# Optimization experiments

Hardware: AMD Instinct MI355X
Metric: run time of the kernel (lower is better)

Reference implementation:

```python
import jax, jax.numpy as jnp
import numpy as np

D_MODEL = 256
D_HID = 128
EPS = 1e-5
MASK_VALUE = -10000.0


def _layer_norm(x, scale, bias):
    mu = jnp.mean(x, axis=-1, keepdims=True)
    var = jnp.mean(jnp.square(x - mu), axis=-1, keepdims=True)
    return (x - mu) * jax.lax.rsqrt(var + EPS) * scale + bias


def setup_inputs() -> dict:
    key = jax.random.key(0)
    ks = jax.random.split(key, 8)
    B, S = 32, 1024
    std = 0.02
    return {
        "x": jax.random.normal(ks[0], (B, S, D_MODEL), dtype=jnp.float32),
        "ln1_scale": jnp.ones((D_MODEL,), jnp.float32),
        "ln1_bias": jnp.zeros((D_MODEL,), jnp.float32),
        "w_qkv": jax.random.normal(ks[1], (D_MODEL, 3 * D_MODEL), jnp.float32) * std,
        "b_qkv": jnp.zeros((3 * D_MODEL,), jnp.float32),
        "w_proj": jax.random.normal(ks[2], (D_MODEL, D_MODEL), jnp.float32) * std,
        "b_proj": jnp.zeros((D_MODEL,), jnp.float32),
        "ln2_scale": jnp.ones((D_MODEL,), jnp.float32),
        "ln2_bias": jnp.zeros((D_MODEL,), jnp.float32),
        "w_fc1": jax.random.normal(ks[3], (D_MODEL, D_HID), jnp.float32) * std,
        "b_fc1": jnp.zeros((D_HID,), jnp.float32),
        "w_fc2": jax.random.normal(ks[4], (D_HID, D_MODEL), jnp.float32) * std,
        "b_fc2": jnp.zeros((D_MODEL,), jnp.float32),
    }


def reference(x, ln1_scale, ln1_bias, w_qkv, b_qkv, w_proj, b_proj,
              ln2_scale, ln2_bias, w_fc1, b_fc1, w_fc2, b_fc2):
    B, S, D = x.shape
    # --- pre-LN self-attention ---
    residual = x
    h = _layer_norm(x, ln1_scale, ln1_bias)
    qkv = h @ w_qkv + b_qkv                       # [B, S, 3D]
    q, k, v = jnp.split(qkv, 3, axis=2)           # each [B, S, D]; 1 head, head_dim=D
    scale = 1.0 / jnp.sqrt(jnp.asarray(D, x.dtype))
    scores = jnp.einsum('bqd,bkd->bqk', q, k) * scale   # [B, S, S]
    causal = jnp.tril(jnp.ones((S, S), dtype=bool))
    scores = jnp.where(causal[None, :, :], scores, MASK_VALUE)
    attn = jax.nn.softmax(scores, axis=-1)        # dropout is identity (eval mode)
    out = jnp.einsum('bqk,bkd->bqd', attn, v)     # [B, S, D]
    out = out @ w_proj + b_proj
    x = out + residual
    # --- pre-LN MLP ---
    residual = x
    h = _layer_norm(x, ln2_scale, ln2_bias)
    h = jax.nn.relu(h @ w_fc1 + b_fc1)
    h = h @ w_fc2 + b_fc2
    return h + residual
```

## Files before the change

### kernel.cpp

```cpp
#include <hip/hip_runtime.h>
#include <hip/hip_bf16.h>

#define D_MODEL 256
#define D_HID   128
#define SEQ     1024
#define NBATCH  32
#define NROWS   (NBATCH * SEQ)
#define MASKV   -10000.0f
#define EPSLN   1e-5f

typedef unsigned short u16;
using bf16x8 = __attribute__((ext_vector_type(8))) short;
using f32x4  = __attribute__((ext_vector_type(4))) float;

union U8 { uint4 v; u16 s[8]; };

__device__ __forceinline__ float bf2f(u16 u) {
    unsigned int x = ((unsigned int)u) << 16;
    return __uint_as_float(x);
}
__device__ __forceinline__ u16 f2bf(float f) {
    unsigned int u = __float_as_uint(f);
    u += 0x7fff + ((u >> 16) & 1);
    return (u16)(u >> 16);
}
__device__ __forceinline__ void load4(const float* p, float* f) {
    float4 a = *(const float4*)p;
    f[0] = a.x; f[1] = a.y; f[2] = a.z; f[3] = a.w;
}
__device__ __forceinline__ void load4(const u16* p, float* f) {
    ushort4 v = *(const ushort4*)p;
    f[0] = bf2f(v.x); f[1] = bf2f(v.y); f[2] = bf2f(v.z); f[3] = bf2f(v.w);
}
__device__ __forceinline__ void gload16(const u16* g, u16* l) {
    __builtin_amdgcn_global_load_lds(
        (const __attribute__((address_space(1))) void*)g,
        (__attribute__((address_space(3))) void*)l, 16, 0, 0);
}

template <int CTRL>
__device__ __forceinline__ float dpp_mov(float v) {
    return __int_as_float(__builtin_amdgcn_update_dpp(
        0, __float_as_int(v), CTRL, 0xf, 0xf, true));
}
__device__ __forceinline__ float red16_max(float v) {
    v = fmaxf(v, dpp_mov<0xB1>(v));
    v = fmaxf(v, dpp_mov<0x4E>(v));
    v = fmaxf(v, dpp_mov<0x141>(v));
    v = fmaxf(v, dpp_mov<0x140>(v));
    return v;
}
__device__ __forceinline__ float red16_sum(float v) {
    v += dpp_mov<0xB1>(v);
    v += dpp_mov<0x4E>(v);
    v += dpp_mov<0x141>(v);
    v += dpp_mov<0x140>(v);
    return v;
}

__global__ __launch_bounds__(256) void transpose_weights(
    const float* __restrict__ wqkv, u16* __restrict__ wqkvT,
    const float* __restrict__ wproj, u16* __restrict__ wprojT,
    const float* __restrict__ wfc1, u16* __restrict__ wfc1T,
    const float* __restrict__ wfc2, u16* __restrict__ wfc2T) {
    int tid = blockIdx.x * 256 + threadIdx.x;
    int stride = gridDim.x * 256;
    for (int i = tid; i < 768 * 256; i += stride) {
        int n = i >> 8, k = i & 255;
        wqkvT[i] = f2bf(wqkv[k * 768 + n]);
    }
    for (int i = tid; i < 256 * 256; i += stride) {
        int n = i >> 8, k = i & 255;
        wprojT[i] = f2bf(wproj[k * 256 + n]);
    }
    for (int i = tid; i < 128 * 256; i += stride) {
        int n = i >> 8, k = i & 255;
        wfc1T[i] = f2bf(wfc1[k * 128 + n]);
    }
    for (int i = tid; i < 256 * 128; i += stride) {
        int n = i >> 7, k = i & 127;
        wfc2T[i] = f2bf(wfc2[k * 256 + n]);
    }
}

template <typename TX>
__global__ __launch_bounds__(256) void ln_fused(
    const TX* __restrict__ x, const float* __restrict__ gamma,
    const float* __restrict__ beta, u16* __restrict__ out) {
    int wave = threadIdx.x >> 6, lane = threadIdx.x & 63;
    int row = blockIdx.x * 4 + wave;
    float f[4];
    load4(x + (size_t)row * D_MODEL + lane * 4, f);
    float s  = f[0] + f[1] + f[2] + f[3];
    float sq = f[0] * f[0] + f[1] * f[1] + f[2] * f[2] + f[3] * f[3];
    #pragma unroll
    for (int off = 1; off < 64; off <<= 1) {
        s  += __shfl_xor(s, off);
        sq += __shfl_xor(sq, off);
    }
    float mu   = s * (1.0f / 256.0f);
    float var  = sq * (1.0f / 256.0f) - mu * mu;
    float rstd = rsqrtf(var + EPSLN);
    float g[4], be[4];
    load4(gamma + lane * 4, g);
    load4(beta + lane * 4, be);
    ushort4 o;
    o.x = f2bf((f[0] - mu) * rstd * g[0] + be[0]);
    o.y = f2bf((f[1] - mu) * rstd * g[1] + be[1]);
    o.z = f2bf((f[2] - mu) * rstd * g[2] + be[2]);
    o.w = f2bf((f[3] - mu) * rstd * g[3] + be[3]);
    *(ushort4*)(out + (size_t)row * D_MODEL + lane * 4) = o;
}

#define GT2_ELEMS (2 * 128 * 128)

template <int K>
__device__ __forceinline__ void gemm_tile2(
    const u16* __restrict__ A, const u16* __restrict__ BT,
    int m0, int n0, u16* lds, f32x4 acc[4][4]) {
    u16* ldsA = lds;
    u16* ldsB = lds + 128 * 128;
    const int tid = threadIdx.x;
    const int lane = tid & 63, wave = tid >> 6;
    const int wr = (wave >> 1) * 64, wc = (wave & 1) * 64;
    const int row = lane & 15, quad = lane >> 4;

    for (int ks = 0; ks < K; ks += 128) {
        __syncthreads();
        #pragma unroll
        for (int i = 0; i < 8; i++) {
            int blk = i * 4 + wave;
            int B = (blk << 10) + lane * 16;
            int r = B >> 8;
            int cb = (B & 255) ^ ((r & 7) << 4);
            gload16(A + (size_t)(m0 + r) * K + ks + (cb >> 1),
                    ldsA + (blk << 9));
            gload16(BT + (size_t)(n0 + r) * K + ks + (cb >> 1),
                    ldsB + (blk << 9));
        }
        __syncthreads();
        #pragma unroll
        for (int k0 = 0; k0 < 128; k0 += 32) {
            bf16x8 a[4], b[4];
            #pragma unroll
            for (int mi = 0; mi < 4; mi++) {
                int rr = wr + mi * 16 + row;
                a[mi] = *(const bf16x8*)(ldsA + rr * 128 +
                         ((k0 + quad * 8) ^ ((rr & 7) << 3)));
            }
            #pragma unroll
            for (int nj = 0; nj < 4; nj++) {
                int rr = wc + nj * 16 + row;
                b[nj] = *(const bf16x8*)(ldsB + rr * 128 +
                         ((k0 + quad * 8) ^ ((rr & 7) << 3)));
            }
            #pragma unroll
            for (int mi = 0; mi < 4; mi++)
                #pragma unroll
                for (int nj = 0; nj < 4; nj++)
                    acc[mi][nj] = __builtin_amdgcn_mfma_f32_16x16x32_bf16(
                        a[mi], b[nj], acc[mi][nj], 0, 0, 0);
        }
    }
}

#define ZERO_ACC4(acc)                                       \
    _Pragma("unroll") for (int i_ = 0; i_ < 4; i_++)         \
    _Pragma("unroll") for (int j_ = 0; j_ < 4; j_++)         \
    _Pragma("unroll") for (int e_ = 0; e_ < 4; e_++) acc[i_][j_][e_] = 0.0f;

#define EPILOG_IDX4                                          \
    int lane = threadIdx.x & 63, wave = threadIdx.x >> 6;    \
    int wr = (wave >> 1) * 64, wc = (wave & 1) * 64;         \
    int row = lane & 15, quad = lane >> 4;

__global__ __launch_bounds__(256) void gemm_qkv(
    const u16* __restrict__ h, const u16* __restrict__ wqkvT,
    const float* __restrict__ b_qkv,
    u16* __restrict__ q, u16* __restrict__ kk, u16* __restrict__ vT) {
    __shared__ u16 lds[GT2_ELEMS];
    f32x4 acc[4][4];
    ZERO_ACC4(acc)
    int m0 = blockIdx.x * 128, n0 = blockIdx.y * 128;
    gemm_tile2<256>(h, wqkvT, m0, n0, lds, acc);
    EPILOG_IDX4
    #pragma unroll
    for (int mi = 0; mi < 4; mi++) {
        #pragma unroll
        for (int nj = 0; nj < 4; nj++) {
            int gn = n0 + wc + nj * 16 + row;
            float bias = b_qkv[gn];
            int gm = m0 + wr + mi * 16 + quad * 4;
            if (gn < 256) {
                #pragma unroll
                for (int r = 0; r < 4; r++)
                    q[(size_t)(gm + r) * 256 + gn] =
                        f2bf((acc[mi][nj][r] + bias) * 0.0625f);
            } else if (gn < 512) {
                int col = gn - 256;
                #pragma unroll
                for (int r = 0; r < 4; r++)
                    kk[(size_t)(gm + r) * 256 + col] = f2bf(acc[mi][nj][r] + bias);
            } else {
                int d = gn - 512;
                int b = gm >> 10, s = gm & 1023;
                ushort4 pack;
                pack.x = f2bf(acc[mi][nj][0] + bias);
                pack.y = f2bf(acc[mi][nj][1] + bias);
                pack.z = f2bf(acc[mi][nj][2] + bias);
                pack.w = f2bf(acc[mi][nj][3] + bias);
                *(ushort4*)(vT + ((size_t)(b * 256 + d) << 10) + s) = pack;
            }
        }
    }
}

__global__ __launch_bounds__(256) void gemm_proj(
    const u16* __restrict__ ao, const u16* __restrict__ wprojT,
    const float* __restrict__ b_proj, const float* __restrict__ x_in,
    u16* __restrict__ x2) {
    __shared__ u16 lds[GT2_ELEMS];
    f32x4 acc[4][4];
    ZERO_ACC4(acc)
    int m0 = blockIdx.x * 128, n0 = blockIdx.y * 128;
    gemm_tile2<256>(ao, wprojT, m0, n0, lds, acc);
    EPILOG_IDX4
    #pragma unroll
    for (int mi = 0; mi < 4; mi++)
        #pragma unroll
        for (int nj = 0; nj < 4; nj++) {
            int gn = n0 + wc + nj * 16 + row;
            float bias = b_proj[gn];
            int gm = m0 + wr + mi * 16 + quad * 4;
            #pragma unroll
            for (int r = 0; r < 4; r++) {
                size_t idx = (size_t)(gm + r) * 256 + gn;
                x2[idx] = f2bf(acc[mi][nj][r] + bias + x_in[idx]);
            }
        }
}

__global__ __launch_bounds__(256) void gemm_mlp(
    const u16* __restrict__ x2, const float* __restrict__ g2,
    const float* __restrict__ be2,
    const u16* __restrict__ wfc1T, const float* __restrict__ b_fc1,
    const u16* __restrict__ wfc2T, const float* __restrict__ b_fc2,
    float* __restrict__ out) {
    __shared__ u16 lds[65536];
    u16* ldsB1 = lds + 32768;
    u16* ldsA1 = lds + 49152;
    const int tid = threadIdx.x;
    const int lane = tid & 63, wave = tid >> 6;
    const int rowl = lane & 15, quad = lane >> 4;
    const int wr = (wave >> 1) * 64, wc = (wave & 1) * 64;
    const int m0 = blockIdx.x * 128;

    #pragma unroll
    for (int i = 0; i < 16; i++) {
        int blk = i * 4 + wave;
        int B = (blk << 10) + lane * 16;
        int r = B >> 9;
        int cb = (B & 511) ^ ((r & 7) << 4);
        gload16(x2 + (size_t)(m0 + r) * 256 + (cb >> 1), lds + (B >> 1));
    }
    #pragma unroll
    for (int i = 0; i < 8; i++) {
        int blk = i * 4 + wave;
        int B = (blk << 10) + lane * 16;
        int r = B >> 8;
        int cb = (B & 255) ^ ((r & 7) << 4);
        gload16(wfc1T + (size_t)r * 256 + 0 + (cb >> 1), ldsB1 + (B >> 1));
    }
    __syncthreads();

    {
        float4 g4  = *(const float4*)(g2 + lane * 4);
        float4 be4 = *(const float4*)(be2 + lane * 4);
        #pragma unroll 4
        for (int i = 0; i < 32; i++) {
            int r = wave + i * 4;
            char* p = (char*)lds + r * 512 + ((lane * 8) ^ ((r & 7) << 4));
            ushort4 v = *(ushort4*)p;
            float f0 = bf2f(v.x), f1 = bf2f(v.y), f2v = bf2f(v.z), f3 = bf2f(v.w);
            float s  = f0 + f1 + f2v + f3;
            float sq = f0*f0 + f1*f1 + f2v*f2v + f3*f3;
            s = red16_sum(s);   s += __shfl_xor(s, 16);   s += __shfl_xor(s, 32);
            sq = red16_sum(sq); sq += __shfl_xor(sq, 16); sq += __shfl_xor(sq, 32);
            float mu   = s * (1.0f / 256.0f);
            float var  = sq * (1.0f / 256.0f) - mu * mu;
            float rstd = rsqrtf(var + EPSLN);
            ushort4 o;
            o.x = f2bf((f0  - mu) * rstd * g4.x + be4.x);
            o.y = f2bf((f1  - mu) * rstd * g4.y + be4.y);
            o.z = f2bf((f2v - mu) * rstd * g4.z + be4.z);
            o.w = f2bf((f3  - mu) * rstd * g4.w + be4.w);
            *(ushort4*)p = o;
        }
    }
    __syncthreads();

    f32x4 acc1[4][4];
    ZERO_ACC4(acc1)
    #pragma unroll
    for (int ks = 0; ks < 256; ks += 128) {
        if (ks) {
            __syncthreads();
            #pragma unroll
            for (int i = 0; i < 8; i++) {
                int blk = i * 4 + wave;
                int B = (blk << 10) + lane * 16;
                int r = B >> 8;
                int cb = (B & 255) ^ ((r & 7) << 4);
                gload16(wfc1T + (size_t)r * 256 + ks + (cb >> 1),
                        ldsB1 + (B >> 1));
            }
            __syncthreads();
        }
        #pragma unroll
        for (int k0 = 0; k0 < 128; k0 += 32) {
            bf16x8 a[4], b[4];
            #pragma unroll
            for (int mi = 0; mi < 4; mi++) {
                int rr = wr + mi * 16 + rowl;
                a[mi] = *(const bf16x8*)((const char*)lds + rr * 512 +
                         ((((ks + k0 + quad * 8) << 1)) ^ ((rr & 7) << 4)));
            }
            #pragma unroll
            for (int nj = 0; nj < 4; nj++) {
                int rb = wc + nj * 16 + rowl;
                b[nj] = *(const bf16x8*)((const char*)ldsB1 + rb * 256 +
                         ((((k0 + quad * 8) << 1)) ^ ((rb & 7) << 4)));
            }
            #pragma unroll
            for (int mi = 0; mi < 4; mi++)
                #pragma unroll
                for (int nj = 0; nj < 4; nj++)
                    acc1[mi][nj] = __builtin_amdgcn_mfma_f32_16x16x32_bf16(
                        a[mi], b[nj], acc1[mi][nj], 0, 0, 0);
        }
    }
    #pragma unroll
    for (int mi = 0; mi < 4; mi++)
        #pragma unroll
        for (int nj = 0; nj < 4; nj++) {
            int gn_l = wc + nj * 16 + rowl;
            float bias = b_fc1[gn_l];
            #pragma unroll
            for (int r = 0; r < 4; r++) {
                int gm_l = wr + mi * 16 + quad * 4 + r;
                *(u16*)((char*)ldsA1 + gm_l * 256 +
                        (((gn_l << 1)) ^ ((gm_l & 7) << 4))) =
                    f2bf(fmaxf(acc1[mi][nj][r] + bias, 0.0f));
            }
        }
    __syncthreads();

    #pragma unroll
    for (int i = 0; i < 16; i++) {
        int blk = i * 4 + wave;
        int B = (blk << 10) + lane * 16;
        int r = B >> 8;
        int cb = (B & 255) ^ ((r & 7) << 4);
        gload16(wfc2T + (size_t)r * 128 + (cb >> 1), lds + (B >> 1));
    }
    __syncthreads();

    const int wc2 = (wave & 1) * 128;
    f32x4 acc2[4][8];
    #pragma unroll
    for (int mi = 0; mi < 4; mi++)
        #pragma unroll
        for (int nj = 0; nj < 8; nj++)
            #pragma unroll
            for (int e = 0; e < 4; e++) acc2[mi][nj][e] = 0.0f;
    #pragma unroll
    for (int k0 = 0; k0 < 128; k0 += 32) {
        bf16x8 a[4], b[8];
        #pragma unroll
        for (int mi = 0; mi < 4; mi++) {
            int rr = wr + mi * 16 + rowl;
            a[mi] = *(const bf16x8*)((const char*)ldsA1 + rr * 256 +
                     ((((k0 + quad * 8) << 1)) ^ ((rr & 7) << 4)));
        }
        #pragma unroll
        for (int nj = 0; nj < 8; nj++) {
            int rb = wc2 + nj * 16 + rowl;
            b[nj] = *(const bf16x8*)((const char*)lds + rb * 256 +
                     ((((k0 + quad * 8) << 1)) ^ ((rb & 7) << 4)));
        }
        #pragma unroll
        for (int mi = 0; mi < 4; mi++)
            #pragma unroll
            for (int nj = 0; nj < 8; nj++)
                acc2[mi][nj] = __builtin_amdgcn_mfma_f32_16x16x32_bf16(
                    a[mi], b[nj], acc2[mi][nj], 0, 0, 0);
    }
    #pragma unroll
    for (int mi = 0; mi < 4; mi++)
        #pragma unroll
        for (int nj = 0; nj < 8; nj++) {
            int gn = wc2 + nj * 16 + rowl;
            float bias = b_fc2[gn];
            int gm = m0 + wr + mi * 16 + quad * 4;
            #pragma unroll
            for (int r = 0; r < 4; r++) {
                size_t idx = (size_t)(gm + r) * 256 + gn;
                out[idx] = acc2[mi][nj][r] + bias + bf2f(x2[idx]);
            }
        }
}

__constant__ unsigned char WQT[24] = {7,15,15,14,14,6,13,13,12,12,5,11,
                                      11,10,10,4,9,9,8,8,3,2,1,0};
__constant__ unsigned char WH[24]  = {2,0,1,0,1,2,0,1,0,1,2,0,
                                      1,0,1,2,0,1,0,1,2,2,2,2};

__global__ __launch_bounds__(256) void attn_kernel(
    const u16* __restrict__ q, const u16* __restrict__ k,
    const u16* __restrict__ vT, u16* __restrict__ ao,
    u16* __restrict__ part, float* __restrict__ ml) {
    __shared__ u16 k_lds[2][32 * 256];
    __shared__ u16 v_lds[2][256 * 32];
    __shared__ u16 p_lds[4][16 * 40];

    int j = blockIdx.x;
    int b = j & 31, w = j >> 5;
    int qt = WQT[w], hh = WH[w];
    int lo, hi;
    if (hh == 2) { lo = 0; hi = 2 * qt + 2; }
    else         { lo = hh * (qt + 1); hi = lo + qt + 1; }

    int tid = threadIdx.x;
    int lane = tid & 63, wave = tid >> 6;
    int row = lane & 15, quad = lane >> 4;
    int q0 = qt * 64;
    int qrow0 = q0 + wave * 16;

    const u16* qb = q + ((size_t)b << 10) * 256;
    const u16* kb = k + ((size_t)b << 10) * 256;
    const u16* vb = vT + (((size_t)b * 256) << 10);

    const int kxor = (row & 7) << 3;
    const int vxor = (row & 6) << 2;

    bf16x8 qf[8];
    #pragma unroll
    for (int kf = 0; kf < 8; kf++)
        qf[kf] = *(const bf16x8*)(qb + (size_t)(qrow0 + row) * 256 + kf * 32 + quad * 8);

    f32x4 o[16];
    #pragma unroll
    for (int n = 0; n < 16; n++)
        #pragma unroll
        for (int e = 0; e < 4; e++) o[n][e] = 0.0f;
    float m_i[4], l_i[4];
    #pragma unroll
    for (int r = 0; r < 4; r++) { m_i[r] = -1e30f; l_i[r] = 0.0f; }

    int wlast = 2 * qt + (wave >> 1);

    auto stage = [&](int bf, int kt) {
        int k0 = kt << 5;
        #pragma unroll
        for (int c = 0; c < 4; c++) {
            int blk = wave * 4 + c;
            int B = (blk << 10) + lane * 16;
            int rk = B >> 9;
            int ck = (B & 511) ^ ((rk & 7) << 4);
            gload16(kb + (size_t)(k0 + rk) * 256 + (ck >> 1),
                    &k_lds[bf][blk << 9]);
            int rv = B >> 6;
            int cv = (B & 63) ^ ((rv & 6) << 3);
            gload16(vb + ((size_t)rv << 10) + k0 + (cv >> 1),
                    &v_lds[bf][blk << 9]);
        }
    };

    stage(0, lo);
    __syncthreads();

    for (int kt = lo; kt < hi; kt++) {
        int cur = (kt - lo) & 1;
        if (kt + 1 < hi) stage(cur ^ 1, kt + 1);
        if (kt <= wlast) {
            const u16* kl = k_lds[cur];
            const u16* vl = v_lds[cur];

            f32x4 sf[2];
            #pragma unroll
            for (int jn = 0; jn < 2; jn++)
                #pragma unroll
                for (int e = 0; e < 4; e++) sf[jn][e] = 0.0f;
            __builtin_amdgcn_s_setprio(1);
            #pragma unroll
            for (int kf = 0; kf < 8; kf++)
                #pragma unroll
                for (int jn = 0; jn < 2; jn++) {
                    bf16x8 bfrag = *(const bf16x8*)(kl +
                        ((((jn * 16 + row) * 256) + kf * 32 + quad * 8) ^ kxor));
                    sf[jn] = __builtin_amdgcn_mfma_f32_16x16x32_bf16(
                        qf[kf], bfrag, sf[jn], 0, 0, 0);
                }
            __builtin_amdgcn_s_setprio(0);

            int kk0 = kt * 32;
            bool diag = (kt == wlast);
            int qrow = qrow0 + quad * 4;
            float sv[2][4];
            #pragma unroll
            for (int jn = 0; jn < 2; jn++)
                #pragma unroll
                for (int r = 0; r < 4; r++) {
                    float v = sf[jn][r];
                    if (diag && (kk0 + jn * 16 + row > qrow + r)) v = MASKV;
                    sv[jn][r] = v;
                }

            float pmax[4];
            int need = 0;
            #pragma unroll
            for (int r = 0; r < 4; r++) {
                pmax[r] = red16_max(fmaxf(sv[0][r], sv[1][r]));
                need |= (pmax[r] > m_i[r] + 8.0f) ? 1 : 0;
            }
            if (__any(need)) {
                #pragma unroll
                for (int r = 0; r < 4; r++) {
                    float mnew = fmaxf(m_i[r], pmax[r]);
                    float al = __expf(m_i[r] - mnew);
                    m_i[r] = mnew;
                    l_i[r] *= al;
                    #pragma unroll
                    for (int n = 0; n < 16; n++) o[n][r] *= al;
                }
            }
            #pragma unroll
            for (int r = 0; r < 4; r++) {
                float ps = 0.0f;
                #pragma unroll
                for (int jn = 0; jn < 2; jn++) {
                    sv[jn][r] = __expf(sv[jn][r] - m_i[r]);
                    ps += sv[jn][r];
                }
                l_i[r] += red16_sum(ps);
            }

            u16* pw = p_lds[wave];
            #pragma unroll
            for (int jn = 0; jn < 2; jn++)
                #pragma unroll
                for (int r = 0; r < 4; r++)
                    pw[(quad * 4 + r) * 40 + jn * 16 + row] = f2bf(sv[jn][r]);
            bf16x8 pf = *(const bf16x8*)(pw + row * 40 + quad * 8);

            __builtin_amdgcn_s_setprio(1);
            #pragma unroll
            for (int n = 0; n < 16; n++) {
                bf16x8 bv = *(const bf16x8*)(vl +
                    ((((n * 16 + row) * 32) + quad * 8) ^ vxor));
                o[n] = __builtin_amdgcn_mfma_f32_16x16x32_bf16(pf, bv, o[n], 0, 0, 0);
            }
            __builtin_amdgcn_s_setprio(0);
        }
        __syncthreads();
    }

    if (hh == 2) {
        float inv[4];
        #pragma unroll
        for (int r = 0; r < 4; r++) inv[r] = 1.0f / l_i[r];
        u16* aob = ao + (((size_t)b << 10) + qrow0) * 256;
        #pragma unroll
        for (int r = 0; r < 4; r++)
            #pragma unroll
            for (int n = 0; n < 16; n++)
                aob[(size_t)(quad * 4 + r) * 256 + n * 16 + row] =
                    f2bf(o[n][r] * inv[r]);
    } else {
        int p = (((b << 3) | (qt - 8)) << 1) | hh;
        u16* pb = part + (((size_t)p) << 6) * 256;
        #pragma unroll
        for (int r = 0; r < 4; r++) {
            int rt = wave * 16 + quad * 4 + r;
            #pragma unroll
            for (int n = 0; n < 16; n++)
                pb[(size_t)rt * 256 + n * 16 + row] = f2bf(o[n][r]);
        }
        if (row == 0) {
            #pragma unroll
            for (int r = 0; r < 4; r++) {
                int rt = wave * 16 + quad * 4 + r;
                float2 v2; v2.x = m_i[r]; v2.y = l_i[r];
                *(float2*)(ml + ((size_t)((p << 6) + rt)) * 2) = v2;
            }
        }
    }
}

__global__ __launch_bounds__(256) void attn_merge(
    const u16* __restrict__ part, const float* __restrict__ ml,
    u16* __restrict__ ao) {
    int j = blockIdx.x;
    int b = j >> 3, qi = j & 7;
    int t = threadIdx.x;
    int r = t >> 2, cq = t & 3;
    int pA = j << 1, pB = pA | 1;
    const float* mlA = ml + ((size_t)(pA << 6) + r) * 2;
    const float* mlB = ml + ((size_t)(pB << 6) + r) * 2;
    float mA = mlA[0], lA = mlA[1];
    float mB = mlB[0], lB = mlB[1];
    float m  = fmaxf(mA, mB);
    float eA = __expf(mA - m), eB = __expf(mB - m);
    float inv = 1.0f / (lA * eA + lB * eB);
    float sA = eA * inv, sB = eB * inv;
    const u16* oA = part + (((size_t)(pA << 6) + r) * 256) + cq * 64;
    const u16* oB = part + (((size_t)(pB << 6) + r) * 256) + cq * 64;
    u16* dst = ao + ((size_t)((b << 10) + 512 + (qi << 6) + r)) * 256 + cq * 64;
    #pragma unroll
    for (int u = 0; u < 8; u++) {
        U8 a, bb, o;
        a.v  = *(const uint4*)(oA + u * 8);
        bb.v = *(const uint4*)(oB + u * 8);
        #pragma unroll
        for (int e = 0; e < 8; e++)
            o.s[e] = f2bf(bf2f(a.s[e]) * sA + bf2f(bb.s[e]) * sB);
        *(uint4*)(dst + u * 8) = o.v;
    }
}

extern "C" void kernel_launch(void* const* d_in, const int* in_sizes, int n_in,
                              void* d_out, int out_size, void* d_ws, size_t ws_size,
                              hipStream_t stream) {
    const float* x      = (const float*)d_in[0];
    const float* ln1_s  = (const float*)d_in[1];
    const float* ln1_b  = (const float*)d_in[2];
    const float* w_qkv  = (const float*)d_in[3];
    const float* b_qkv  = (const float*)d_in[4];
    const float* w_proj = (const float*)d_in[5];
    const float* b_proj = (const float*)d_in[6];
    const float* ln2_s  = (const float*)d_in[7];
    const float* ln2_b  = (const float*)d_in[8];
    const float* w_fc1  = (const float*)d_in[9];
    const float* b_fc1  = (const float*)d_in[10];
    const float* w_fc2  = (const float*)d_in[11];
    const float* b_fc2  = (const float*)d_in[12];
    float* out = (float*)d_out;

    u16* h  = (u16*)d_out;
    u16* h2 = h + (size_t)NROWS * 256;

    u16* W = (u16*)d_ws;
    u16* wqkvT  = W;
    u16* wprojT = wqkvT + 196608;
    u16* wfc1T  = wprojT + 65536;
    u16* wfc2T  = wfc1T + 32768;
    u16* buf1   = wfc2T + 32768;
    u16* buf2   = buf1 + (size_t)NROWS * 256;
    u16* buf3   = buf2 + (size_t)NROWS * 256;

    u16*   part  = h;
    float* mlbuf = (float*)h2;

    transpose_weights<<<dim3(64), dim3(256), 0, stream>>>(
        w_qkv, wqkvT, w_proj, wprojT, w_fc1, wfc1T, w_fc2, wfc2T);
    ln_fused<float><<<dim3(NROWS / 4), dim3(256), 0, stream>>>(
        x, ln1_s, ln1_b, h);
    gemm_qkv<<<dim3(NROWS / 128, 6), dim3(256), 0, stream>>>(
        h, wqkvT, b_qkv, buf1, buf2, buf3);
    attn_kernel<<<dim3(768), dim3(256), 0, stream>>>(
        buf1, buf2, buf3, buf1, part, mlbuf);
    attn_merge<<<dim3(256), dim3(256), 0, stream>>>(
        part, mlbuf, buf1);
    gemm_proj<<<dim3(NROWS / 128, 2), dim3(256), 0, stream>>>(
        buf1, wprojT, b_proj, x, buf2);
    gemm_mlp<<<dim3(NROWS / 128), dim3(256), 0, stream>>>(
        buf2, ln2_s, ln2_b, wfc1T, b_fc1, wfc2T, b_fc2, out);
}
```

Measured before the change: 246.4 us.

## Use 128-row query tiles with 512-thread attention blocks and rebalance KV splits

Attention blocks now cover 128 query rows with 8 waves instead of 64 rows with 4, so each staged K/V tile is shared by twice as many query rows. Each thread stages half as many chunks. The work split changes: the first 128-row tile runs unsplit and all later tiles are split into two equal KV halves, giving 480 blocks. The merge kernel, the partial-buffer indexing and the placement of the ml buffer are rewritten to match. The aim is less K/V reload traffic and better load balance, at the cost of larger blocks, higher register pressure under launch_bounds(512,4), and more merge work.

After: 372.5 us. 1.51x slower.

```diff
diff --git a/kernel.cpp b/kernel.cpp
--- a/kernel.cpp
+++ b/kernel.cpp
@@ -410,31 +410,29 @@
         }
 }
 
-__constant__ unsigned char WQT[24] = {7,15,15,14,14,6,13,13,12,12,5,11,
-                                      11,10,10,4,9,9,8,8,3,2,1,0};
-__constant__ unsigned char WH[24]  = {2,0,1,0,1,2,0,1,0,1,2,0,
-                                      1,0,1,2,0,1,0,1,2,2,2,2};
-
-__global__ __launch_bounds__(256) void attn_kernel(
+__constant__ unsigned char CQT[15] = {7,6,6,5,5,4,4,7, 0,1,1,2,2,3,3};
+__constant__ unsigned char CH[15]  = {0,0,1,0,1,0,1,1, 2,0,1,0,1,0,1};
+
+__global__ __launch_bounds__(512, 4) void attn_kernel(
     const u16* __restrict__ q, const u16* __restrict__ k,
     const u16* __restrict__ vT, u16* __restrict__ ao,
     u16* __restrict__ part, float* __restrict__ ml) {
     __shared__ u16 k_lds[2][32 * 256];
     __shared__ u16 v_lds[2][256 * 32];
-    __shared__ u16 p_lds[4][16 * 40];
+    __shared__ u16 p_lds[8][16 * 40];
 
     int j = blockIdx.x;
-    int b = j & 31, w = j >> 5;
-    int qt = WQT[w], hh = WH[w];
+    int b = j & 31, c = j >> 5;
+    int qt = CQT[c], ch = CH[c];
+    int span = 2 * qt + 2;
     int lo, hi;
-    if (hh == 2) { lo = 0; hi = 2 * qt + 2; }
-    else         { lo = hh * (qt + 1); hi = lo + qt + 1; }
+    if (ch == 2) { lo = 0; hi = 4; }
+    else         { lo = ch * span; hi = lo + span; }
 
     int tid = threadIdx.x;
     int lane = tid & 63, wave = tid >> 6;
     int row = lane & 15, quad = lane >> 4;
-    int q0 = qt * 64;
-    int qrow0 = q0 + wave * 16;
+    int qrow0 = qt * 128 + wave * 16;
 
     const u16* qb = q + ((size_t)b << 10) * 256;
     const u16* kb = k + ((size_t)b << 10) * 256;
@@ -457,13 +455,13 @@
     #pragma unroll
     for (int r = 0; r < 4; r++) { m_i[r] = -1e30f; l_i[r] = 0.0f; }
 
-    int wlast = 2 * qt + (wave >> 1);
+    int wlast = 4 * qt + (wave >> 1);
 
     auto stage = [&](int bf, int kt) {
         int k0 = kt << 5;
         #pragma unroll
-        for (int c = 0; c < 4; c++) {
-            int blk = wave * 4 + c;
+        for (int cc = 0; cc < 2; cc++) {
+            int blk = wave * 2 + cc;
             int B = (blk << 10) + lane * 16;
             int rk = B >> 9;
             int ck = (B & 511) ^ ((rk & 7) << 4);
@@ -565,7 +563,7 @@
         __syncthreads();
     }
 
-    if (hh == 2) {
+    if (ch == 2) {
         float inv[4];
         #pragma unroll
         for (int r = 0; r < 4; r++) inv[r] = 1.0f / l_i[r];
@@ -577,8 +575,8 @@
                 aob[(size_t)(quad * 4 + r) * 256 + n * 16 + row] =
                     f2bf(o[n][r] * inv[r]);
     } else {
-        int p = (((b << 3) | (qt - 8)) << 1) | hh;
-        u16* pb = part + (((size_t)p) << 6) * 256;
+        int pq = b * 7 + (qt - 1);
+        u16* pb = part + ((size_t)(ch * 224 + pq) << 15);
         #pragma unroll
         for (int r = 0; r < 4; r++) {
             int rt = wave * 16 + quad * 4 + r;
@@ -587,11 +585,12 @@
                 pb[(size_t)rt * 256 + n * 16 + row] = f2bf(o[n][r]);
         }
         if (row == 0) {
+            int p = pq * 2 + ch;
             #pragma unroll
             for (int r = 0; r < 4; r++) {
                 int rt = wave * 16 + quad * 4 + r;
                 float2 v2; v2.x = m_i[r]; v2.y = l_i[r];
-                *(float2*)(ml + ((size_t)((p << 6) + rt)) * 2) = v2;
+                *(float2*)(ml + ((size_t)(p * 128 + rt)) * 2) = v2;
             }
         }
     }
@@ -601,21 +600,23 @@
     const u16* __restrict__ part, const float* __restrict__ ml,
     u16* __restrict__ ao) {
     int j = blockIdx.x;
-    int b = j >> 3, qi = j & 7;
+    int b = j / 14, rem = j - b * 14;
+    int qt = (rem >> 1) + 1, rh = rem & 1;
     int t = threadIdx.x;
     int r = t >> 2, cq = t & 3;
-    int pA = j << 1, pB = pA | 1;
-    const float* mlA = ml + ((size_t)(pA << 6) + r) * 2;
-    const float* mlB = ml + ((size_t)(pB << 6) + r) * 2;
+    int rt = rh * 64 + r;
+    int pq = b * 7 + (qt - 1);
+    const float* mlA = ml + ((size_t)((pq * 2 + 0) * 128 + rt)) * 2;
+    const float* mlB = ml + ((size_t)((pq * 2 + 1) * 128 + rt)) * 2;
     float mA = mlA[0], lA = mlA[1];
     float mB = mlB[0], lB = mlB[1];
     float m  = fmaxf(mA, mB);
     float eA = __expf(mA - m), eB = __expf(mB - m);
     float inv = 1.0f / (lA * eA + lB * eB);
     float sA = eA * inv, sB = eB * inv;
-    const u16* oA = part + (((size_t)(pA << 6) + r) * 256) + cq * 64;
-    const u16* oB = part + (((size_t)(pB << 6) + r) * 256) + cq * 64;
-    u16* dst = ao + ((size_t)((b << 10) + 512 + (qi << 6) + r)) * 256 + cq * 64;
+    const u16* oA = part + ((size_t)pq << 15) + (size_t)rt * 256 + cq * 64;
+    const u16* oB = part + ((size_t)(224 + pq) << 15) + (size_t)rt * 256 + cq * 64;
+    u16* dst = ao + ((size_t)((b << 10) + qt * 128 + rt)) * 256 + cq * 64;
     #pragma unroll
     for (int u = 0; u < 8; u++) {
         U8 a, bb, o;
@@ -646,8 +647,7 @@
     const float* b_fc2  = (const float*)d_in[12];
     float* out = (float*)d_out;
 
-    u16* h  = (u16*)d_out;
-    u16* h2 = h + (size_t)NROWS * 256;
+    u16* h = (u16*)d_out;
 
     u16* W = (u16*)d_ws;
     u16* wqkvT  = W;
@@ -659,7 +659,7 @@
     u16* buf3   = buf2 + (size_t)NROWS * 256;
 
     u16*   part  = h;
-    float* mlbuf = (float*)h2;
+    float* mlbuf = (float*)d_out + 7340032;
 
     transpose_weights<<<dim3(64), dim3(256), 0, stream>>>(
         w_qkv, wqkvT, w_proj, wprojT, w_fc1, wfc1T, w_fc2, wfc2T);
@@ -667,9 +667,9 @@
         x, ln1_s, ln1_b, h);
     gemm_qkv<<<dim3(NROWS / 128, 6), dim3(256), 0, stream>>>(
         h, wqkvT, b_qkv, buf1, buf2, buf3);
-    attn_kernel<<<dim3(768), dim3(256), 0, stream>>>(
+    attn_kernel<<<dim3(480), dim3(512), 0, stream>>>(
         buf1, buf2, buf3, buf1, part, mlbuf);
-    attn_merge<<<dim3(256), dim3(256), 0, stream>>>(
+    attn_merge<<<dim3(448), dim3(256), 0, stream>>>(
         part, mlbuf, buf1);
     gemm_proj<<<dim3(NROWS / 128, 2), dim3(256), 0, stream>>>(
         buf1, wprojT, b_proj, x, buf2);
```
